# Performance work log

Measured on AMD Instinct MI355X. Metric: run time of the kernel, lower is better.

Reference implementation:

```python
import jax, jax.numpy as jnp
import numpy as np

B, T, V, H, E, MAX_OOV = 128, 200, 50257, 256, 128, 50


def setup_inputs() -> dict:
    key = jax.random.key(0)
    ks = jax.random.split(key, 17)
    s = 0.05  # param scale
    return {
        "decoder_input": jax.random.randint(ks[0], (B, 1), 0, V),
        "encoder_outputs": jax.random.normal(ks[1], (B, T, 2 * H), jnp.float32),
        "encoder_idxs": jax.random.randint(ks[2], (B, T), 0, V),
        "prev_state": jax.random.normal(ks[3], (1, B, H), jnp.float32),
        "selective_read": jax.random.normal(ks[4], (B, 1, 2 * H), jnp.float32) * s,
        "step": 1,
        "emb": jax.random.normal(ks[5], (V, E), jnp.float32) * s,
        "W_ih": jax.random.normal(ks[6], (3 * H, E + 2 * H), jnp.float32) * s,
        "W_hh": jax.random.normal(ks[7], (3 * H, H), jnp.float32) * s,
        "b_ih": jax.random.normal(ks[8], (3 * H,), jnp.float32) * s,
        "b_hh": jax.random.normal(ks[9], (3 * H,), jnp.float32) * s,
        "Wi_w": jax.random.normal(ks[10], (H, 2 * H), jnp.float32) * s,
        "Wi_b": jax.random.normal(ks[11], (H,), jnp.float32) * s,
        "Wg_w": jax.random.normal(ks[12], (V, H), jnp.float32) * s,
        "Wg_b": jax.random.normal(ks[13], (V,), jnp.float32) * s,
        "Wc_w": jax.random.normal(ks[14], (H, 2 * H), jnp.float32) * s,
        "Wc_b": jax.random.normal(ks[15], (H,), jnp.float32) * s,
    }


def _gru_cell(x, h, W_ih, W_hh, b_ih, b_hh):
    # torch GRUCell math, gate order r,z,n
    gi = x @ W_ih.T + b_ih
    gh = h @ W_hh.T + b_hh
    i_r, i_z, i_n = jnp.split(gi, 3, axis=-1)
    h_r, h_z, h_n = jnp.split(gh, 3, axis=-1)
    r = jax.nn.sigmoid(i_r + h_r)
    z = jax.nn.sigmoid(i_z + h_z)
    n = jnp.tanh(i_n + r * h_n)
    return (1.0 - z) * n + z * h


def reference(decoder_input, encoder_outputs, encoder_idxs, prev_state, selective_read,
              step, emb, W_ih, W_hh, b_ih, b_hh, Wi_w, Wi_b, Wg_w, Wg_b, Wc_w, Wc_b):
    dtype = encoder_outputs.dtype
    if step == 0:
        prev_state = (encoder_outputs[:, -1] @ Wi_w.T + Wi_b)[None]      # 1,B,H
        selective_read = jnp.zeros((B, 1, 2 * H), dtype)
    embedded = emb[decoder_input[:, 0]]                                   # B,E
    gru_in = jnp.concatenate([selective_read[:, 0], embedded], axis=-1)   # B,2H+E
    decode_hidden = _gru_cell(gru_in, prev_state[0], W_ih, W_hh, b_ih, b_hh)  # B,H

    score_g = decode_hidden @ Wg_w.T + Wg_b                               # B,V
    enc_proj = jnp.tanh(jnp.einsum('bte,he->bth', encoder_outputs, Wc_w) + Wc_b)  # B,T,H
    score_c = jnp.tanh(jnp.einsum('bth,bh->bt', enc_proj, decode_hidden))         # B,T
    score_c = score_c + jnp.where(encoder_idxs == 0, -10000.0, 0.0).astype(dtype)

    probs = jax.nn.softmax(jnp.concatenate([score_g, score_c], axis=1), axis=1)   # B,V+T
    prob_g, prob_c = probs[:, :V], probs[:, V:]
    prob_g = jnp.concatenate([prob_g, jnp.full((B, MAX_OOV), 1e-4, dtype)], axis=1)  # B,V+oov

    # copy-distribution aggregation: scatter-add prob_c by vocab id (replaces one-hot bmm)
    prob_c_to_g = jnp.zeros((B, V + MAX_OOV), dtype).at[
        jnp.arange(B)[:, None], encoder_idxs].add(prob_c)
    prob_out = (prob_c_to_g + prob_g)[:, None, :]                          # B,1,V+oov

    # selective read for next step
    match = (encoder_idxs == decoder_input).astype(dtype)                  # B,T
    tot = match.sum(axis=1, keepdims=True)
    match = jnp.where(tot > 1, match / tot, match)
    prob_appeared = prob_c * match
    selective_read_new = jnp.einsum('bt,bte->be', prob_appeared, encoder_outputs)[:, None, :]  # B,1,2H
    return prob_out, decode_hidden, selective_read_new
```

## Files before the change

### kernel.cpp

```cpp
#include <hip/hip_runtime.h>

typedef __bf16 bf16;
typedef __bf16 bf16x8 __attribute__((ext_vector_type(8)));
typedef float f32x4 __attribute__((ext_vector_type(4)));

#define B_ 128
#define T_ 200
#define V_ 50257
#define H_ 256
#define E_ 128
#define OOV_ 50
#define VO_ 50307
#define PSTR 3144
#define NBG 112
#define NTB 7
#define GBG 449
#define TILES_G 3143

__device__ __forceinline__ float sigmoid_(float x) { return 1.0f / (1.0f + __expf(-x)); }
__device__ __forceinline__ float tanh_(float x) { return 1.0f - 2.0f / (__expf(2.0f * x) + 1.0f); }

__global__ void k_cvt_wc(const float* Wc_w, bf16* WcPack) {
    int gid = blockIdx.x * 256 + threadIdx.x;
    int n = gid >> 7;
    int k4 = gid & 127;
    int k = k4 * 4;
    float4 v = *(const float4*)(Wc_w + n * 512 + k);
    int kstep = k >> 5, kin = k & 31;
    int q = kin >> 3, j0 = kin & 7;
    int r = n & 15, nt = n >> 4;
    int lane = q * 16 + r;
    bf16* d = WcPack + (((nt * 16 + kstep) * 64) + lane) * 8 + j0;
    d[0] = (bf16)v.x; d[1] = (bf16)v.y; d[2] = (bf16)v.z; d[3] = (bf16)v.w;
}

__global__ void k_prep(const int* step_p, const float* enc, const float* prev,
                       const float* selread, const int* dec, const float* emb,
                       const float* Wi_w, const float* Wi_b,
                       float* hT, float* ginT) {
    int b = blockIdx.x, t = threadIdx.x;
    int step = step_p[0];
    float h;
    if (step == 0) {
        float acc = Wi_b[t];
        const float* er = enc + (b * T_ + (T_ - 1)) * 512;
        const float* wr = Wi_w + t * 512;
        for (int k = 0; k < 512; ++k) acc += er[k] * wr[k];
        h = acc;
    } else {
        h = prev[b * H_ + t];
    }
    hT[t * B_ + b] = h;
    for (int k = t; k < 512; k += 256)
        ginT[k * B_ + b] = (step == 0) ? 0.0f : selread[b * 512 + k];
    if (t < E_)
        ginT[(512 + t) * B_ + b] = emb[dec[b] * E_ + t];
}

__global__ void k_gemm_gru(const float* W_ih, const float* b_ih,
                           const float* W_hh, const float* b_hh,
                           const float* ginT, const float* hT,
                           float* giT, float* ghT) {
    int g = blockIdx.x * 256 + threadIdx.x;
    int r = g >> 7, b = g & 127;
    float acc = b_ih[r];
    const float* w = W_ih + r * 640;
#pragma unroll 8
    for (int k = 0; k < 640; ++k) acc += w[k] * ginT[k * B_ + b];
    giT[r * B_ + b] = acc;
    float acc2 = b_hh[r];
    const float* w2 = W_hh + r * 256;
#pragma unroll 8
    for (int k = 0; k < 256; ++k) acc2 += w2[k] * hT[k * B_ + b];
    ghT[r * B_ + b] = acc2;
}

__global__ void k_gru_cell(const float* giT, const float* ghT, const float* hT,
                           float* out_dh, bf16* Apack) {
    int b = blockIdx.x, j = threadIdx.x;
    float ir = giT[j * B_ + b], iz = giT[(256 + j) * B_ + b], in_ = giT[(512 + j) * B_ + b];
    float hr = ghT[j * B_ + b], hz = ghT[(256 + j) * B_ + b], hn = ghT[(512 + j) * B_ + b];
    float hp = hT[j * B_ + b];
    float r = sigmoid_(ir + hr);
    float z = sigmoid_(iz + hz);
    float n = tanh_(in_ + r * hn);
    float h = (1.0f - z) * n + z * hp;
    out_dh[b * H_ + j] = h;
    int mt = b >> 4, rr = b & 15, ks = j >> 5, q = (j >> 3) & 3, jj = j & 7;
    Apack[(((mt * 8 + ks) * 64) + (q * 16 + rr)) * 8 + jj] = (bf16)h;
}

__global__ __launch_bounds__(256, 2) void k_score_g(const bf16* Apack, const float* Wg_w,
                                                    const float* Wg_b, float* out_prob,
                                                    float* pg_part) {
    __shared__ bf16 Bs[NBG * 264];
    int tid = threadIdx.x;
    int blk = blockIdx.x;
    int n0 = blk * NBG;
#pragma unroll
    for (int j = 0; j < 28; ++j) {
        int f = tid + j * 256;
        int row = f >> 6;
        int c4 = f & 63;
        int n = n0 + row;
        float4 v = (n < V_) ? *(const float4*)(Wg_w + n * 256 + c4 * 4)
                            : float4{0.f, 0.f, 0.f, 0.f};
        bf16* d = Bs + row * 264 + c4 * 4;
        d[0] = (bf16)v.x; d[1] = (bf16)v.y; d[2] = (bf16)v.z; d[3] = (bf16)v.w;
    }
    int w = tid >> 6, lane = tid & 63;
    int r = lane & 15, q = lane >> 4;
    bf16x8 a[2][8];
#pragma unroll
    for (int p = 0; p < 2; ++p)
#pragma unroll
        for (int ks = 0; ks < 8; ++ks)
            a[p][ks] = *(const bf16x8*)(Apack + (((2 * w + p) * 8 + ks) * 64 + lane) * 8);
    __syncthreads();
    f32x4 acc[14];
#pragma unroll
    for (int i = 0; i < 14; ++i) acc[i] = (f32x4){0.f, 0.f, 0.f, 0.f};
#pragma unroll
    for (int ks = 0; ks < 8; ++ks) {
#pragma unroll
        for (int nt = 0; nt < NTB; ++nt) {
            bf16x8 bfr = *(const bf16x8*)(Bs + (nt * 16 + r) * 264 + ks * 32 + q * 8);
            acc[nt * 2]     = __builtin_amdgcn_mfma_f32_16x16x32_bf16(a[0][ks], bfr, acc[nt * 2], 0, 0, 0);
            acc[nt * 2 + 1] = __builtin_amdgcn_mfma_f32_16x16x32_bf16(a[1][ks], bfr, acc[nt * 2 + 1], 0, 0, 0);
        }
    }
#pragma unroll
    for (int nt = 0; nt < NTB; ++nt) {
        int n = n0 + nt * 16 + r;
        bool valid = n < V_;
        float wgb = valid ? Wg_b[n] : 0.0f;
#pragma unroll
        for (int p = 0; p < 2; ++p) {
#pragma unroll
            for (int rg = 0; rg < 4; ++rg) {
                int row = (2 * w + p) * 16 + q * 4 + rg;
                float e = valid ? __expf(acc[nt * 2 + p][rg] + wgb) : 0.0f;
                if (valid) out_prob[row * VO_ + n] = e;
                float sred = e;
                sred += __shfl_xor(sred, 1);
                sred += __shfl_xor(sred, 2);
                sred += __shfl_xor(sred, 4);
                sred += __shfl_xor(sred, 8);
                if (r == 0) pg_part[row * PSTR + blk * NTB + nt] = sred;
            }
        }
    }
}

__global__ __launch_bounds__(256) void k_proj_c(const float* enc, const bf16* WcPack,
                                                const float* Wc_b, const float* dh,
                                                const int* idxs, float* expc) {
    __shared__ bf16 As[64 * 264];
    __shared__ float sred[64 * 4];
    int tid = threadIdx.x;
    int m0 = blockIdx.x * 64;
    int w = tid >> 6, lane = tid & 63;
    int r = lane & 15, q = lane >> 4;
    f32x4 acc[16];
#pragma unroll
    for (int i = 0; i < 16; ++i) acc[i] = (f32x4){0.f, 0.f, 0.f, 0.f};
    for (int half = 0; half < 2; ++half) {
        __syncthreads();
#pragma unroll
        for (int j = 0; j < 16; ++j) {
            int f = tid + j * 256;
            int row = f >> 6;
            int c4 = f & 63;
            float4 v = *(const float4*)(enc + (m0 + row) * 512 + half * 256 + c4 * 4);
            bf16* d = As + row * 264 + c4 * 4;
            d[0] = (bf16)v.x; d[1] = (bf16)v.y; d[2] = (bf16)v.z; d[3] = (bf16)v.w;
        }
        __syncthreads();
#pragma unroll
        for (int ks = 0; ks < 8; ++ks) {
            int kstep = half * 8 + ks;
            bf16x8 bfr[4];
#pragma unroll
            for (int ntl = 0; ntl < 4; ++ntl)
                bfr[ntl] = *(const bf16x8*)(WcPack + (((w * 4 + ntl) * 16 + kstep) * 64 + lane) * 8);
#pragma unroll
            for (int mt = 0; mt < 4; ++mt) {
                bf16x8 a = *(const bf16x8*)(As + (mt * 16 + r) * 264 + ks * 32 + q * 8);
#pragma unroll
                for (int ntl = 0; ntl < 4; ++ntl)
                    acc[mt * 4 + ntl] = __builtin_amdgcn_mfma_f32_16x16x32_bf16(a, bfr[ntl], acc[mt * 4 + ntl], 0, 0, 0);
            }
        }
    }
#pragma unroll
    for (int mt = 0; mt < 4; ++mt) {
#pragma unroll
        for (int rg = 0; rg < 4; ++rg) {
            int rowl = mt * 16 + q * 4 + rg;
            int row = m0 + rowl;
            int b = row / T_;
            float s = 0.0f;
#pragma unroll
            for (int ntl = 0; ntl < 4; ++ntl) {
                int n = (w * 4 + ntl) * 16 + r;
                float pv = tanh_(acc[mt * 4 + ntl][rg] + Wc_b[n]);
                s += pv * dh[b * H_ + n];
            }
            s += __shfl_xor(s, 1);
            s += __shfl_xor(s, 2);
            s += __shfl_xor(s, 4);
            s += __shfl_xor(s, 8);
            if (r == 0) sred[rowl * 4 + w] = s;
        }
    }
    __syncthreads();
    if (tid < 64) {
        float s = sred[tid * 4] + sred[tid * 4 + 1] + sred[tid * 4 + 2] + sred[tid * 4 + 3];
        int row = m0 + tid;
        int b = row / T_, t = row - b * T_;
        float sc = tanh_(s);
        if (idxs[b * T_ + t] == 0) sc -= 10000.0f;
        expc[row] = __expf(sc);
    }
}

__global__ void k_rowsum(const float* pg_part, const float* expc, float* inv) {
    __shared__ float red[256];
    int b = blockIdx.x, t = threadIdx.x;
    float s = 0.0f;
    for (int nt = t; nt < TILES_G; nt += 256) s += pg_part[b * PSTR + nt];
    if (t < T_) s += expc[b * T_ + t];
    red[t] = s;
    __syncthreads();
    for (int k = 128; k > 0; k >>= 1) {
        if (t < k) red[t] += red[t + k];
        __syncthreads();
    }
    if (t == 0) inv[b] = 1.0f / red[0];
}

__global__ void k_norm(float* out_prob, const float* inv) {
    int i4 = blockIdx.x * 256 + threadIdx.x;
    if (i4 >= (B_ * VO_ / 4)) return;
    float4 vv = ((const float4*)out_prob)[i4];
    float r[4];
    int base = i4 * 4;
#pragma unroll
    for (int c = 0; c < 4; ++c) {
        int idx = base + c;
        int b = idx / VO_;
        int v = idx - b * VO_;
        float x = (c == 0) ? vv.x : (c == 1) ? vv.y : (c == 2) ? vv.z : vv.w;
        r[c] = (v < V_) ? x * inv[b] : 1e-4f;
    }
    ((float4*)out_prob)[i4] = make_float4(r[0], r[1], r[2], r[3]);
}

__global__ void k_scatter_sel(const float* expc, const float* inv, const int* idxs,
                              const int* dec, const float* enc,
                              float* out_prob, float* out_sel) {
    __shared__ float cf[256];
    __shared__ float red[256];
    int b = blockIdx.x, t = threadIdx.x;
    int d = dec[b];
    float iv = inv[b];
    float pc = 0.0f;
    int m = 0;
    if (t < T_) {
        int ix = idxs[b * T_ + t];
        pc = expc[b * T_ + t] * iv;
        atomicAdd(&out_prob[b * VO_ + ix], pc);
        m = (ix == d) ? 1 : 0;
    }
    cf[t] = m ? pc : 0.0f;
    red[t] = m ? 1.0f : 0.0f;
    __syncthreads();
    for (int s = 128; s > 0; s >>= 1) {
        if (t < s) red[t] += red[t + s];
        __syncthreads();
    }
    float tot = red[0];
    float scale = (tot > 1.0f) ? 1.0f / tot : 1.0f;
    float a0 = 0.0f, a1 = 0.0f;
    for (int tt = 0; tt < T_; ++tt) {
        float c = cf[tt];
        if (c != 0.0f) {
            float w = c * scale;
            a0 += w * enc[(b * T_ + tt) * 512 + t];
            a1 += w * enc[(b * T_ + tt) * 512 + t + 256];
        }
    }
    out_sel[b * 512 + t] = a0;
    out_sel[b * 512 + t + 256] = a1;
}

extern "C" void kernel_launch(void* const* d_in, const int* in_sizes, int n_in,
                              void* d_out, int out_size, void* d_ws, size_t ws_size,
                              hipStream_t stream) {
    const int*   dec     = (const int*)d_in[0];
    const float* enc     = (const float*)d_in[1];
    const int*   idxs    = (const int*)d_in[2];
    const float* prev    = (const float*)d_in[3];
    const float* selread = (const float*)d_in[4];
    const int*   step_p  = (const int*)d_in[5];
    const float* emb     = (const float*)d_in[6];
    const float* W_ih    = (const float*)d_in[7];
    const float* W_hh    = (const float*)d_in[8];
    const float* b_ih    = (const float*)d_in[9];
    const float* b_hh    = (const float*)d_in[10];
    const float* Wi_w    = (const float*)d_in[11];
    const float* Wi_b    = (const float*)d_in[12];
    const float* Wg_w    = (const float*)d_in[13];
    const float* Wg_b    = (const float*)d_in[14];
    const float* Wc_w    = (const float*)d_in[15];
    const float* Wc_b    = (const float*)d_in[16];

    float* ws     = (float*)d_ws;
    float* hT     = ws;
    float* ginT   = ws + 32768;
    float* giT    = ws + 114688;
    float* ghT    = ws + 212992;
    float* inv    = ws + 311296;
    float* expc   = ws + 311552;
    float* pgp    = ws + 337152;
    bf16*  Apack  = (bf16*)(ws + 739584);
    bf16*  WcPack = (bf16*)(ws + 755968);

    float* out      = (float*)d_out;
    float* out_prob = out;
    float* out_dh   = out + 6439296;
    float* out_sel  = out + 6439296 + 32768;

    k_cvt_wc<<<128, 256, 0, stream>>>(Wc_w, WcPack);
    k_prep<<<B_, 256, 0, stream>>>(step_p, enc, prev, selread, dec, emb, Wi_w, Wi_b, hT, ginT);
    k_gemm_gru<<<384, 256, 0, stream>>>(W_ih, b_ih, W_hh, b_hh, ginT, hT, giT, ghT);
    k_gru_cell<<<B_, 256, 0, stream>>>(giT, ghT, hT, out_dh, Apack);
    k_score_g<<<GBG, 256, 0, stream>>>(Apack, Wg_w, Wg_b, out_prob, pgp);
    k_proj_c<<<400, 256, 0, stream>>>(enc, WcPack, Wc_b, out_dh, idxs, expc);
    k_rowsum<<<B_, 256, 0, stream>>>(pgp, expc, inv);
    k_norm<<<(B_ * VO_ / 4 + 255) / 256, 256, 0, stream>>>(out_prob, inv);
    k_scatter_sel<<<B_, 256, 0, stream>>>(expc, inv, idxs, dec, enc, out_prob, out_sel);
}
```

Before: 293.8 us.

## Merge vocab and copy GEMMs into one launch, fuse scatter before normalize

Combines the Wc pack and prep kernels into one launch, and the vocab-score GEMM and copy-projection GEMM into a single heterogeneous grid so both run concurrently. The vocab tile shrinks to 80 rows, with occupancy hinted at 3 blocks per CU. Exp results are staged through shared memory for coalesced float4 stores. The row-sum and scatter/selective-read kernels are merged, and the unnormalized copy exps are scattered before the normalize pass so one kernel fewer runs. The GRU GEMV gets four independent accumulators to break the dependency chain.

Measured after the change: 271.3 us. 7.6% less time.

```diff
diff --git a/kernel.cpp b/kernel.cpp
--- a/kernel.cpp
+++ b/kernel.cpp
@@ -11,50 +11,51 @@
 #define E_ 128
 #define OOV_ 50
 #define VO_ 50307
-#define PSTR 3144
-#define NBG 112
-#define NTB 7
-#define GBG 449
-#define TILES_G 3143
+#define NRG 80
+#define NTS 5
+#define GSC 629
+#define TILES_G 3145
+#define PSTR 3152
+#define GPJ 400
 
 __device__ __forceinline__ float sigmoid_(float x) { return 1.0f / (1.0f + __expf(-x)); }
 __device__ __forceinline__ float tanh_(float x) { return 1.0f - 2.0f / (__expf(2.0f * x) + 1.0f); }
 
-__global__ void k_cvt_wc(const float* Wc_w, bf16* WcPack) {
-    int gid = blockIdx.x * 256 + threadIdx.x;
-    int n = gid >> 7;
-    int k4 = gid & 127;
-    int k = k4 * 4;
-    float4 v = *(const float4*)(Wc_w + n * 512 + k);
-    int kstep = k >> 5, kin = k & 31;
-    int q = kin >> 3, j0 = kin & 7;
-    int r = n & 15, nt = n >> 4;
-    int lane = q * 16 + r;
-    bf16* d = WcPack + (((nt * 16 + kstep) * 64) + lane) * 8 + j0;
-    d[0] = (bf16)v.x; d[1] = (bf16)v.y; d[2] = (bf16)v.z; d[3] = (bf16)v.w;
-}
-
-__global__ void k_prep(const int* step_p, const float* enc, const float* prev,
-                       const float* selread, const int* dec, const float* emb,
-                       const float* Wi_w, const float* Wi_b,
-                       float* hT, float* ginT) {
-    int b = blockIdx.x, t = threadIdx.x;
-    int step = step_p[0];
-    float h;
-    if (step == 0) {
-        float acc = Wi_b[t];
-        const float* er = enc + (b * T_ + (T_ - 1)) * 512;
-        const float* wr = Wi_w + t * 512;
-        for (int k = 0; k < 512; ++k) acc += er[k] * wr[k];
-        h = acc;
+__global__ void k_front(const float* Wc_w, bf16* WcPack,
+                        const int* step_p, const float* enc, const float* prev,
+                        const float* selread, const int* dec, const float* emb,
+                        const float* Wi_w, const float* Wi_b,
+                        float* hT, float* ginT) {
+    if (blockIdx.x < 128) {
+        int gid = blockIdx.x * 256 + threadIdx.x;
+        int n = gid >> 7;
+        int k = (gid & 127) * 4;
+        float4 v = *(const float4*)(Wc_w + n * 512 + k);
+        int kstep = k >> 5, kin = k & 31;
+        int q = kin >> 3, j0 = kin & 7;
+        int r = n & 15, nt = n >> 4;
+        int lane = q * 16 + r;
+        bf16* d = WcPack + (((nt * 16 + kstep) * 64) + lane) * 8 + j0;
+        d[0] = (bf16)v.x; d[1] = (bf16)v.y; d[2] = (bf16)v.z; d[3] = (bf16)v.w;
     } else {
-        h = prev[b * H_ + t];
-    }
-    hT[t * B_ + b] = h;
-    for (int k = t; k < 512; k += 256)
-        ginT[k * B_ + b] = (step == 0) ? 0.0f : selread[b * 512 + k];
-    if (t < E_)
-        ginT[(512 + t) * B_ + b] = emb[dec[b] * E_ + t];
+        int b = blockIdx.x - 128, t = threadIdx.x;
+        int step = step_p[0];
+        float h;
+        if (step == 0) {
+            float acc = Wi_b[t];
+            const float* er = enc + (b * T_ + (T_ - 1)) * 512;
+            const float* wr = Wi_w + t * 512;
+            for (int k = 0; k < 512; ++k) acc += er[k] * wr[k];
+            h = acc;
+        } else {
+            h = prev[b * H_ + t];
+        }
+        hT[t * B_ + b] = h;
+        for (int k = t; k < 512; k += 256)
+            ginT[k * B_ + b] = (step == 0) ? 0.0f : selread[b * 512 + k];
+        if (t < E_)
+            ginT[(512 + t) * B_ + b] = emb[dec[b] * E_ + t];
+    }
 }
 
 __global__ void k_gemm_gru(const float* W_ih, const float* b_ih,
@@ -63,16 +64,26 @@
                            float* giT, float* ghT) {
     int g = blockIdx.x * 256 + threadIdx.x;
     int r = g >> 7, b = g & 127;
-    float acc = b_ih[r];
     const float* w = W_ih + r * 640;
-#pragma unroll 8
-    for (int k = 0; k < 640; ++k) acc += w[k] * ginT[k * B_ + b];
-    giT[r * B_ + b] = acc;
-    float acc2 = b_hh[r];
+    float a0 = 0.f, a1 = 0.f, a2 = 0.f, a3 = 0.f;
+#pragma unroll 4
+    for (int k = 0; k < 640; k += 4) {
+        a0 += w[k]     * ginT[k * B_ + b];
+        a1 += w[k + 1] * ginT[(k + 1) * B_ + b];
+        a2 += w[k + 2] * ginT[(k + 2) * B_ + b];
+        a3 += w[k + 3] * ginT[(k + 3) * B_ + b];
+    }
+    giT[r * B_ + b] = b_ih[r] + ((a0 + a1) + (a2 + a3));
     const float* w2 = W_hh + r * 256;
-#pragma unroll 8
-    for (int k = 0; k < 256; ++k) acc2 += w2[k] * hT[k * B_ + b];
-    ghT[r * B_ + b] = acc2;
+    float c0 = 0.f, c1 = 0.f, c2 = 0.f, c3 = 0.f;
+#pragma unroll 4
+    for (int k = 0; k < 256; k += 4) {
+        c0 += w2[k]     * hT[k * B_ + b];
+        c1 += w2[k + 1] * hT[(k + 1) * B_ + b];
+        c2 += w2[k + 2] * hT[(k + 2) * B_ + b];
+        c3 += w2[k + 3] * hT[(k + 3) * B_ + b];
+    }
+    ghT[r * B_ + b] = b_hh[r] + ((c0 + c1) + (c2 + c3));
 }
 
 __global__ void k_gru_cell(const float* giT, const float* ghT, const float* hT,
@@ -90,153 +101,229 @@
     Apack[(((mt * 8 + ks) * 64) + (q * 16 + rr)) * 8 + jj] = (bf16)h;
 }
 
-__global__ __launch_bounds__(256, 2) void k_score_g(const bf16* Apack, const float* Wg_w,
-                                                    const float* Wg_b, float* out_prob,
-                                                    float* pg_part) {
-    __shared__ bf16 Bs[NBG * 264];
+__global__ __launch_bounds__(256, 3) void k_mm(const bf16* Apack, const float* Wg_w,
+                                               const float* Wg_b, const float* enc,
+                                               const bf16* WcPack, const float* Wc_b,
+                                               const float* dh, const int* idxs,
+                                               float* out_prob, float* pg_part, float* expc) {
+    __shared__ unsigned char smem[43008];
     int tid = threadIdx.x;
-    int blk = blockIdx.x;
-    int n0 = blk * NBG;
-#pragma unroll
-    for (int j = 0; j < 28; ++j) {
-        int f = tid + j * 256;
-        int row = f >> 6;
-        int c4 = f & 63;
-        int n = n0 + row;
-        float4 v = (n < V_) ? *(const float4*)(Wg_w + n * 256 + c4 * 4)
-                            : float4{0.f, 0.f, 0.f, 0.f};
-        bf16* d = Bs + row * 264 + c4 * 4;
-        d[0] = (bf16)v.x; d[1] = (bf16)v.y; d[2] = (bf16)v.z; d[3] = (bf16)v.w;
-    }
     int w = tid >> 6, lane = tid & 63;
     int r = lane & 15, q = lane >> 4;
-    bf16x8 a[2][8];
-#pragma unroll
-    for (int p = 0; p < 2; ++p)
-#pragma unroll
-        for (int ks = 0; ks < 8; ++ks)
-            a[p][ks] = *(const bf16x8*)(Apack + (((2 * w + p) * 8 + ks) * 64 + lane) * 8);
-    __syncthreads();
-    f32x4 acc[14];
-#pragma unroll
-    for (int i = 0; i < 14; ++i) acc[i] = (f32x4){0.f, 0.f, 0.f, 0.f};
-#pragma unroll
-    for (int ks = 0; ks < 8; ++ks) {
-#pragma unroll
-        for (int nt = 0; nt < NTB; ++nt) {
-            bf16x8 bfr = *(const bf16x8*)(Bs + (nt * 16 + r) * 264 + ks * 32 + q * 8);
-            acc[nt * 2]     = __builtin_amdgcn_mfma_f32_16x16x32_bf16(a[0][ks], bfr, acc[nt * 2], 0, 0, 0);
-            acc[nt * 2 + 1] = __builtin_amdgcn_mfma_f32_16x16x32_bf16(a[1][ks], bfr, acc[nt * 2 + 1], 0, 0, 0);
-        }
-    }
-#pragma unroll
-    for (int nt = 0; nt < NTB; ++nt) {
-        int n = n0 + nt * 16 + r;
-        bool valid = n < V_;
-        float wgb = valid ? Wg_b[n] : 0.0f;
-#pragma unroll
-        for (int p = 0; p < 2; ++p) {
+    if (blockIdx.x < GSC) {
+        int blk = blockIdx.x;
+        int n0 = blk * NRG;
+        bf16* Bs = (bf16*)smem;
+#pragma unroll
+        for (int ph = 0; ph < 2; ++ph) {
+            float4 tmp[10];
+#pragma unroll
+            for (int j = 0; j < 10; ++j) {
+                int f = (ph * 10 + j) * 256 + tid;
+                int row = f >> 6, c4 = f & 63;
+                int n = n0 + row;
+                tmp[j] = (n < V_) ? *(const float4*)(Wg_w + n * 256 + c4 * 4)
+                                  : float4{0.f, 0.f, 0.f, 0.f};
+            }
+#pragma unroll
+            for (int j = 0; j < 10; ++j) {
+                int f = (ph * 10 + j) * 256 + tid;
+                int row = f >> 6, c4 = f & 63;
+                bf16* d = Bs + row * 264 + c4 * 4;
+                d[0] = (bf16)tmp[j].x; d[1] = (bf16)tmp[j].y;
+                d[2] = (bf16)tmp[j].z; d[3] = (bf16)tmp[j].w;
+            }
+        }
+        bf16x8 a[2][8];
+#pragma unroll
+        for (int p = 0; p < 2; ++p)
+#pragma unroll
+            for (int ks = 0; ks < 8; ++ks)
+                a[p][ks] = *(const bf16x8*)(Apack + ((2 * w + p) * 8 + ks) * 512 + lane * 8);
+        __syncthreads();
+        f32x4 acc[10];
+#pragma unroll
+        for (int i = 0; i < 10; ++i) acc[i] = (f32x4){0.f, 0.f, 0.f, 0.f};
+#pragma unroll
+        for (int ks = 0; ks < 8; ++ks) {
+#pragma unroll
+            for (int nt = 0; nt < NTS; ++nt) {
+                bf16x8 bfr = *(const bf16x8*)(Bs + (nt * 16 + r) * 264 + ks * 32 + q * 8);
+                acc[nt * 2]     = __builtin_amdgcn_mfma_f32_16x16x32_bf16(a[0][ks], bfr, acc[nt * 2], 0, 0, 0);
+                acc[nt * 2 + 1] = __builtin_amdgcn_mfma_f32_16x16x32_bf16(a[1][ks], bfr, acc[nt * 2 + 1], 0, 0, 0);
+            }
+        }
+        __syncthreads();
+        float* Tr = (float*)smem;
+#pragma unroll
+        for (int nt = 0; nt < NTS; ++nt) {
+            int n = n0 + nt * 16 + r;
+            bool valid = n < V_;
+            float wgb = valid ? Wg_b[n] : 0.0f;
+#pragma unroll
+            for (int p = 0; p < 2; ++p) {
+#pragma unroll
+                for (int rg = 0; rg < 4; ++rg) {
+                    int row = (2 * w + p) * 16 + q * 4 + rg;
+                    float e = valid ? __expf(acc[nt * 2 + p][rg] + wgb) : 0.0f;
+                    Tr[row * 84 + nt * 16 + r] = e;
+                    float sred = e;
+                    sred += __shfl_xor(sred, 1);
+                    sred += __shfl_xor(sred, 2);
+                    sred += __shfl_xor(sred, 4);
+                    sred += __shfl_xor(sred, 8);
+                    if (r == 0) pg_part[row * PSTR + blk * NTS + nt] = sred;
+                }
+            }
+        }
+        __syncthreads();
+        if (blk < GSC - 1) {
+#pragma unroll
+            for (int rnd = 0; rnd < 10; ++rnd) {
+                int f = rnd * 256 + tid;
+                int row = (f * 3277) >> 16;
+                int c4 = f - row * 20;
+                float4 v = *(const float4*)(Tr + row * 84 + c4 * 4);
+                *(float4*)(out_prob + row * VO_ + n0 + c4 * 4) = v;
+            }
+        } else {
+#pragma unroll
+            for (int rnd = 0; rnd < 10; ++rnd) {
+                int f = rnd * 256 + tid;
+                int row = (f * 3277) >> 16;
+                int c4 = f - row * 20;
+#pragma unroll
+                for (int i = 0; i < 4; ++i) {
+                    int n = n0 + c4 * 4 + i;
+                    if (n < V_) out_prob[row * VO_ + n] = Tr[row * 84 + c4 * 4 + i];
+                }
+            }
+        }
+    } else {
+        int pblk = blockIdx.x - GSC;
+        int m0 = pblk * 64;
+        bf16* As = (bf16*)smem;
+        float* sred = (float*)(smem + 33792);
+        f32x4 acc[16];
+#pragma unroll
+        for (int i = 0; i < 16; ++i) acc[i] = (f32x4){0.f, 0.f, 0.f, 0.f};
+        for (int half = 0; half < 2; ++half) {
+            __syncthreads();
+#pragma unroll
+            for (int ph = 0; ph < 2; ++ph) {
+                float4 tmp[8];
+#pragma unroll
+                for (int j = 0; j < 8; ++j) {
+                    int f = (ph * 8 + j) * 256 + tid;
+                    int row = f >> 6, c4 = f & 63;
+                    tmp[j] = *(const float4*)(enc + (m0 + row) * 512 + half * 256 + c4 * 4);
+                }
+#pragma unroll
+                for (int j = 0; j < 8; ++j) {
+                    int f = (ph * 8 + j) * 256 + tid;
+                    int row = f >> 6, c4 = f & 63;
+                    bf16* d = As + row * 264 + c4 * 4;
+                    d[0] = (bf16)tmp[j].x; d[1] = (bf16)tmp[j].y;
+                    d[2] = (bf16)tmp[j].z; d[3] = (bf16)tmp[j].w;
+                }
+            }
+            __syncthreads();
+#pragma unroll
+            for (int ks = 0; ks < 8; ++ks) {
+                int kstep = half * 8 + ks;
+                bf16x8 bfr[4];
+#pragma unroll
+                for (int ntl = 0; ntl < 4; ++ntl)
+                    bfr[ntl] = *(const bf16x8*)(WcPack + (((w * 4 + ntl) * 16 + kstep) * 64 + lane) * 8);
+#pragma unroll
+                for (int mt = 0; mt < 4; ++mt) {
+                    bf16x8 a = *(const bf16x8*)(As + (mt * 16 + r) * 264 + ks * 32 + q * 8);
+#pragma unroll
+                    for (int ntl = 0; ntl < 4; ++ntl)
+                        acc[mt * 4 + ntl] = __builtin_amdgcn_mfma_f32_16x16x32_bf16(a, bfr[ntl], acc[mt * 4 + ntl], 0, 0, 0);
+                }
+            }
+        }
+#pragma unroll
+        for (int mt = 0; mt < 4; ++mt) {
 #pragma unroll
             for (int rg = 0; rg < 4; ++rg) {
-                int row = (2 * w + p) * 16 + q * 4 + rg;
-                float e = valid ? __expf(acc[nt * 2 + p][rg] + wgb) : 0.0f;
-                if (valid) out_prob[row * VO_ + n] = e;
-                float sred = e;
-                sred += __shfl_xor(sred, 1);
-                sred += __shfl_xor(sred, 2);
-                sred += __shfl_xor(sred, 4);
-                sred += __shfl_xor(sred, 8);
-                if (r == 0) pg_part[row * PSTR + blk * NTB + nt] = sred;
-            }
-        }
-    }
-}
-
-__global__ __launch_bounds__(256) void k_proj_c(const float* enc, const bf16* WcPack,
-                                                const float* Wc_b, const float* dh,
-                                                const int* idxs, float* expc) {
-    __shared__ bf16 As[64 * 264];
-    __shared__ float sred[64 * 4];
-    int tid = threadIdx.x;
-    int m0 = blockIdx.x * 64;
-    int w = tid >> 6, lane = tid & 63;
-    int r = lane & 15, q = lane >> 4;
-    f32x4 acc[16];
-#pragma unroll
-    for (int i = 0; i < 16; ++i) acc[i] = (f32x4){0.f, 0.f, 0.f, 0.f};
-    for (int half = 0; half < 2; ++half) {
-        __syncthreads();
-#pragma unroll
-        for (int j = 0; j < 16; ++j) {
-            int f = tid + j * 256;
-            int row = f >> 6;
-            int c4 = f & 63;
-            float4 v = *(const float4*)(enc + (m0 + row) * 512 + half * 256 + c4 * 4);
-            bf16* d = As + row * 264 + c4 * 4;
-            d[0] = (bf16)v.x; d[1] = (bf16)v.y; d[2] = (bf16)v.z; d[3] = (bf16)v.w;
-        }
-        __syncthreads();
-#pragma unroll
-        for (int ks = 0; ks < 8; ++ks) {
-            int kstep = half * 8 + ks;
-            bf16x8 bfr[4];
-#pragma unroll
-            for (int ntl = 0; ntl < 4; ++ntl)
-                bfr[ntl] = *(const bf16x8*)(WcPack + (((w * 4 + ntl) * 16 + kstep) * 64 + lane) * 8);
-#pragma unroll
-            for (int mt = 0; mt < 4; ++mt) {
-                bf16x8 a = *(const bf16x8*)(As + (mt * 16 + r) * 264 + ks * 32 + q * 8);
-#pragma unroll
-                for (int ntl = 0; ntl < 4; ++ntl)
-                    acc[mt * 4 + ntl] = __builtin_amdgcn_mfma_f32_16x16x32_bf16(a, bfr[ntl], acc[mt * 4 + ntl], 0, 0, 0);
-            }
-        }
-    }
-#pragma unroll
-    for (int mt = 0; mt < 4; ++mt) {
-#pragma unroll
-        for (int rg = 0; rg < 4; ++rg) {
-            int rowl = mt * 16 + q * 4 + rg;
-            int row = m0 + rowl;
-            int b = row / T_;
-            float s = 0.0f;
-#pragma unroll
-            for (int ntl = 0; ntl < 4; ++ntl) {
-                int n = (w * 4 + ntl) * 16 + r;
-                float pv = tanh_(acc[mt * 4 + ntl][rg] + Wc_b[n]);
-                s += pv * dh[b * H_ + n];
-            }
-            s += __shfl_xor(s, 1);
-            s += __shfl_xor(s, 2);
-            s += __shfl_xor(s, 4);
-            s += __shfl_xor(s, 8);
-            if (r == 0) sred[rowl * 4 + w] = s;
-        }
-    }
-    __syncthreads();
-    if (tid < 64) {
-        float s = sred[tid * 4] + sred[tid * 4 + 1] + sred[tid * 4 + 2] + sred[tid * 4 + 3];
-        int row = m0 + tid;
-        int b = row / T_, t = row - b * T_;
-        float sc = tanh_(s);
-        if (idxs[b * T_ + t] == 0) sc -= 10000.0f;
-        expc[row] = __expf(sc);
-    }
-}
-
-__global__ void k_rowsum(const float* pg_part, const float* expc, float* inv) {
+                int rowl = mt * 16 + q * 4 + rg;
+                int row = m0 + rowl;
+                int b = row / T_;
+                float s = 0.0f;
+#pragma unroll
+                for (int ntl = 0; ntl < 4; ++ntl) {
+                    int n = (w * 4 + ntl) * 16 + r;
+                    float pv = tanh_(acc[mt * 4 + ntl][rg] + Wc_b[n]);
+                    s += pv * dh[b * H_ + n];
+                }
+                s += __shfl_xor(s, 1);
+                s += __shfl_xor(s, 2);
+                s += __shfl_xor(s, 4);
+                s += __shfl_xor(s, 8);
+                if (r == 0) sred[rowl * 4 + w] = s;
+            }
+        }
+        __syncthreads();
+        if (tid < 64) {
+            float s = sred[tid * 4] + sred[tid * 4 + 1] + sred[tid * 4 + 2] + sred[tid * 4 + 3];
+            int row = m0 + tid;
+            int b = row / T_, t = row - b * T_;
+            float sc = tanh_(s);
+            if (idxs[b * T_ + t] == 0) sc -= 10000.0f;
+            expc[row] = __expf(sc);
+        }
+    }
+}
+
+__global__ void k_red_scatter(const float* pg_part, const float* expc_, const int* idxs,
+                              const int* dec, const float* enc, float* inv_out,
+                              float* out_prob, float* out_sel) {
     __shared__ float red[256];
+    __shared__ float cf[256];
     int b = blockIdx.x, t = threadIdx.x;
     float s = 0.0f;
-    for (int nt = t; nt < TILES_G; nt += 256) s += pg_part[b * PSTR + nt];
-    if (t < T_) s += expc[b * T_ + t];
+    for (int i = t; i < TILES_G; i += 256) s += pg_part[b * PSTR + i];
+    if (t < T_) s += expc_[b * T_ + t];
     red[t] = s;
     __syncthreads();
     for (int k = 128; k > 0; k >>= 1) {
         if (t < k) red[t] += red[t + k];
         __syncthreads();
     }
-    if (t == 0) inv[b] = 1.0f / red[0];
+    float iv = 1.0f / red[0];
+    if (t == 0) inv_out[b] = iv;
+    __syncthreads();
+    int d = dec[b];
+    float ec = 0.0f;
+    int m = 0;
+    if (t < T_) {
+        int ix = idxs[b * T_ + t];
+        ec = expc_[b * T_ + t];
+        atomicAdd(&out_prob[b * VO_ + ix], ec);
+        m = (ix == d) ? 1 : 0;
+    }
+    cf[t] = m ? ec * iv : 0.0f;
+    red[t] = m ? 1.0f : 0.0f;
+    __syncthreads();
+    for (int k = 128; k > 0; k >>= 1) {
+        if (t < k) red[t] += red[t + k];
+        __syncthreads();
+    }
+    float tot = red[0];
+    float scale = (tot > 1.0f) ? 1.0f / tot : 1.0f;
+    float a0 = 0.0f, a1 = 0.0f;
+    for (int tt = 0; tt < T_; ++tt) {
+        float c = cf[tt];
+        if (c != 0.0f) {
+            float wgt = c * scale;
+            a0 += wgt * enc[(b * T_ + tt) * 512 + t];
+            a1 += wgt * enc[(b * T_ + tt) * 512 + t + 256];
+        }
+    }
+    out_sel[b * 512 + t] = a0;
+    out_sel[b * 512 + t + 256] = a1;
 }
 
 __global__ void k_norm(float* out_prob, const float* inv) {
@@ -254,44 +341,6 @@
         r[c] = (v < V_) ? x * inv[b] : 1e-4f;
     }
     ((float4*)out_prob)[i4] = make_float4(r[0], r[1], r[2], r[3]);
-}
-
-__global__ void k_scatter_sel(const float* expc, const float* inv, const int* idxs,
-                              const int* dec, const float* enc,
-                              float* out_prob, float* out_sel) {
-    __shared__ float cf[256];
-    __shared__ float red[256];
-    int b = blockIdx.x, t = threadIdx.x;
-    int d = dec[b];
-    float iv = inv[b];
-    float pc = 0.0f;
-    int m = 0;
-    if (t < T_) {
-        int ix = idxs[b * T_ + t];
-        pc = expc[b * T_ + t] * iv;
-        atomicAdd(&out_prob[b * VO_ + ix], pc);
-        m = (ix == d) ? 1 : 0;
-    }
-    cf[t] = m ? pc : 0.0f;
-    red[t] = m ? 1.0f : 0.0f;
-    __syncthreads();
-    for (int s = 128; s > 0; s >>= 1) {
-        if (t < s) red[t] += red[t + s];
-        __syncthreads();
-    }
-    float tot = red[0];
-    float scale = (tot > 1.0f) ? 1.0f / tot : 1.0f;
-    float a0 = 0.0f, a1 = 0.0f;
-    for (int tt = 0; tt < T_; ++tt) {
-        float c = cf[tt];
-        if (c != 0.0f) {
-            float w = c * scale;
-            a0 += w * enc[(b * T_ + tt) * 512 + t];
-            a1 += w * enc[(b * T_ + tt) * 512 + t + 256];
-        }
-    }
-    out_sel[b * 512 + t] = a0;
-    out_sel[b * 512 + t + 256] = a1;
 }
 
 extern "C" void kernel_launch(void* const* d_in, const int* in_sizes, int n_in,
@@ -323,21 +372,20 @@
     float* inv    = ws + 311296;
     float* expc   = ws + 311552;
     float* pgp    = ws + 337152;
-    bf16*  Apack  = (bf16*)(ws + 739584);
-    bf16*  WcPack = (bf16*)(ws + 755968);
+    bf16*  Apack  = (bf16*)(ws + 741376);
+    bf16*  WcPack = (bf16*)(ws + 757760);
 
     float* out      = (float*)d_out;
     float* out_prob = out;
     float* out_dh   = out + 6439296;
     float* out_sel  = out + 6439296 + 32768;
 
-    k_cvt_wc<<<128, 256, 0, stream>>>(Wc_w, WcPack);
-    k_prep<<<B_, 256, 0, stream>>>(step_p, enc, prev, selread, dec, emb, Wi_w, Wi_b, hT, ginT);
+    k_front<<<256, 256, 0, stream>>>(Wc_w, WcPack, step_p, enc, prev, selread, dec,
+                                     emb, Wi_w, Wi_b, hT, ginT);
     k_gemm_gru<<<384, 256, 0, stream>>>(W_ih, b_ih, W_hh, b_hh, ginT, hT, giT, ghT);
     k_gru_cell<<<B_, 256, 0, stream>>>(giT, ghT, hT, out_dh, Apack);
-    k_score_g<<<GBG, 256, 0, stream>>>(Apack, Wg_w, Wg_b, out_prob, pgp);
-    k_proj_c<<<400, 256, 0, stream>>>(enc, WcPack, Wc_b, out_dh, idxs, expc);
-    k_rowsum<<<B_, 256, 0, stream>>>(pgp, expc, inv);
+    k_mm<<<GSC + GPJ, 256, 0, stream>>>(Apack, Wg_w, Wg_b, enc, WcPack, Wc_b,
+                                        out_dh, idxs, out_prob, pgp, expc);
+    k_red_scatter<<<B_, 256, 0, stream>>>(pgp, expc, idxs, dec, enc, inv, out_prob, out_sel);
     k_norm<<<(B_ * VO_ / 4 + 255) / 256, 256, 0, stream>>>(out_prob, inv);
-    k_scatter_sel<<<B_, 256, 0, stream>>>(expc, inv, idxs, dec, enc, out_prob, out_sel);
-}
+}
```
